# Performance work log

Measured on AMD Instinct MI355X. Metric: run time of the kernel, lower is better.

## Reference

```python
import jax, jax.numpy as jnp
import numpy as np

NUM_CLASSES = 81
BACKGROUND = 0
TOP_K = 200
KEEP_TOP_K = 200
CONF_THR = 0.01
NMS_THR = 0.45
B = 32
P = 24564  # SSD512 prior count


def setup_inputs() -> dict:
    key = jax.random.key(0)
    k1, k2, kc, ks = jax.random.split(key, 4)
    loc_data = jax.random.normal(k1, (B, P * 4), jnp.float32) * 0.5
    conf_data = jax.random.uniform(k2, (B, P * NUM_CLASSES), dtype=jnp.float32)
    # priors in corner form [xmin,ymin,xmax,ymax] within [0,1], plus Caffe-style variances
    ctr = jax.random.uniform(kc, (P, 2), minval=0.05, maxval=0.95, dtype=jnp.float32)
    sz = jax.random.uniform(ks, (P, 2), minval=0.02, maxval=0.30, dtype=jnp.float32)
    pboxes = jnp.concatenate([ctr - sz * 0.5, ctr + sz * 0.5], axis=1)  # [P,4]
    variances = jnp.tile(jnp.array([0.1, 0.1, 0.2, 0.2], jnp.float32), (P, 1))  # [P,4]
    prior_data = jnp.stack([pboxes, variances], axis=0).reshape(1, 2, P * 4)
    return {"loc_data": loc_data, "conf_data": conf_data, "prior_data": prior_data}


def _decode(loc, priors, variances):
    # CENTER_SIZE decode, Caffe DetectionOutput convention (priors in corner form).
    pw = priors[:, 2] - priors[:, 0]
    ph = priors[:, 3] - priors[:, 1]
    pcx = (priors[:, 0] + priors[:, 2]) * 0.5
    pcy = (priors[:, 1] + priors[:, 3]) * 0.5
    cx = variances[:, 0] * loc[:, 0] * pw + pcx
    cy = variances[:, 1] * loc[:, 1] * ph + pcy
    w = jnp.exp(variances[:, 2] * loc[:, 2]) * pw
    h = jnp.exp(variances[:, 3] * loc[:, 3]) * ph
    return jnp.stack([cx - w * 0.5, cy - h * 0.5, cx + w * 0.5, cy + h * 0.5], axis=-1)


def _pairwise_iou(b):  # [K,4] -> [K,K]
    x1 = jnp.maximum(b[:, None, 0], b[None, :, 0])
    y1 = jnp.maximum(b[:, None, 1], b[None, :, 1])
    x2 = jnp.minimum(b[:, None, 2], b[None, :, 2])
    y2 = jnp.minimum(b[:, None, 3], b[None, :, 3])
    inter = jnp.clip(x2 - x1, 0.0) * jnp.clip(y2 - y1, 0.0)
    area = jnp.clip(b[:, 2] - b[:, 0], 0.0) * jnp.clip(b[:, 3] - b[:, 1], 0.0)
    union = area[:, None] + area[None, :] - inter
    return inter / jnp.maximum(union, 1e-10)


def _nms_one_class(scores, boxes):
    # scores: [P], boxes: [P,4] -> kept scores [TOP_K], candidate boxes [TOP_K,4]
    s = jnp.where(scores > CONF_THR, scores, -1.0)
    vals, idx = jax.lax.top_k(s, TOP_K)
    cand = boxes[idx]                      # [TOP_K,4]
    iou = _pairwise_iou(cand)              # [TOP_K,TOP_K]
    valid = vals > CONF_THR

    def body(i, carry):
        keep, suppressed = carry
        is_kept = valid[i] & jnp.logical_not(suppressed[i])
        keep = keep.at[i].set(is_kept)
        suppressed = suppressed | (is_kept & (iou[i] > NMS_THR))
        return keep, suppressed

    keep, _ = jax.lax.fori_loop(
        0, TOP_K, body,
        (jnp.zeros((TOP_K,), jnp.bool_), jnp.zeros((TOP_K,), jnp.bool_)))
    kept_scores = jnp.where(keep, vals, 0.0)
    return kept_scores, cand


def _detection_output(loc_data, conf_data, prior_data):
    bsz = loc_data.shape[0]
    nprior = loc_data.shape[1] // 4
    loc = loc_data.reshape(bsz, nprior, 4)
    conf = conf_data.reshape(bsz, nprior, NUM_CLASSES).transpose(0, 2, 1)  # [B,C,P]
    pr = prior_data.reshape(2, nprior, 4)
    priors, variances = pr[0], pr[1]

    decoded = jax.vmap(lambda l: _decode(l, priors, variances))(loc)  # [B,P,4]

    # kill background class
    bg = (jnp.arange(NUM_CLASSES) == BACKGROUND)[None, :, None]
    conf = jnp.where(bg, -1.0, conf)

    nms_bc = jax.vmap(jax.vmap(_nms_one_class, in_axes=(0, None)), in_axes=(0, 0))
    scores, cboxes = nms_bc(conf, decoded)  # [B,C,TOP_K], [B,C,TOP_K,4]

    flat_s = scores.reshape(bsz, NUM_CLASSES * TOP_K)
    top_s, top_i = jax.lax.top_k(flat_s, KEEP_TOP_K)          # [B,KEEP]
    labels = (top_i // TOP_K).astype(jnp.float32)
    flat_b = cboxes.reshape(bsz, NUM_CLASSES * TOP_K, 4)
    top_b = jnp.take_along_axis(flat_b, top_i[..., None], axis=1)  # [B,KEEP,4]

    img_id = jnp.broadcast_to(
        jnp.arange(bsz, dtype=jnp.float32)[:, None], (bsz, KEEP_TOP_K))
    rows = jnp.concatenate(
        [img_id[..., None], labels[..., None], top_s[..., None], top_b], axis=-1)
    rows = jnp.where((top_s > 0.0)[..., None], rows, 0.0)
    return rows[:, None, :, :]  # [B,1,KEEP_TOP_K,7]


def reference(loc_data, conf_data, prior_data):
    return _detection_output(loc_data, conf_data, prior_data)
```

## Files before the change

### kernel.cpp

```cpp
#include <hip/hip_runtime.h>
#include <stdint.h>

typedef uint32_t u32;
typedef uint64_t u64;
typedef uint16_t u16;

#define NCLS 81
#define TOPK 200
#define KEEPK 200
#define CONF_THR 0.01f
#define NMS_THR 0.45f
#define NB 32
#define NP 24564
#define NFLAT (NCLS * TOPK)
#define NPCHUNK 256
#define NCHUNK ((NP + NPCHUNK - 1) / NPCHUNK)
#define CAP 512
#define NBC (NB * NCLS)
#define NGRP (NBC / 4)
#define LCAP 16
#define THRF 0.98828125f

__device__ __forceinline__ u32 fkey(float f) {
  u32 u = __float_as_uint(f);
  return (u & 0x80000000u) ? ~u : (u | 0x80000000u);
}
__device__ __forceinline__ float unfkey(u32 k) {
  u32 u = (k & 0x80000000u) ? (k & 0x7FFFFFFFu) : ~k;
  return __uint_as_float(u);
}

__global__ __launch_bounds__(256) void collect_cands(const float* __restrict__ conf,
                                                     u32* __restrict__ lcnt,
                                                     u64* __restrict__ lcand) {
  __shared__ u32 cnt81[NCLS];
  __shared__ u64 stage[NCLS * LCAP];

  const int tid = threadIdx.x;
  const int blk = blockIdx.x;
  const int b = blk / NCHUNK, chunk = blk % NCHUNK;
  const int p0 = chunk * NPCHUNK;
  const int cntp = min(NPCHUNK, NP - p0);
  const int tot4 = (cntp * NCLS) >> 2;
  const float4* __restrict__ src = (const float4*)(conf + ((size_t)b * NP + p0) * NCLS);

  for (int i = tid; i < NCLS; i += 256) cnt81[i] = 0u;
  __syncthreads();

  auto push = [&](int f, float s) {
    u32 pi = (u32)f / (u32)NCLS;
    u32 c = (u32)f - pi * (u32)NCLS;
    if (c != 0u) {
      u32 sl = atomicAdd(&cnt81[c], 1u);
      if (sl < (u32)LCAP) {
        u32 p = (u32)p0 + pi;
        stage[c * LCAP + sl] = ((u64)fkey(s) << 32) | (u32)(~p);
      }
    }
  };
  auto proc = [&](float4 v, int i4) {
    if (v.x >= THRF) push(i4 * 4 + 0, v.x);
    if (v.y >= THRF) push(i4 * 4 + 1, v.y);
    if (v.z >= THRF) push(i4 * 4 + 2, v.z);
    if (v.w >= THRF) push(i4 * 4 + 3, v.w);
  };

  for (int i = tid; i < tot4; i += 512) {
    int i2 = i + 256;
    bool g2 = i2 < tot4;
    float4 v0 = src[i];
    float4 v1;
    if (g2) v1 = src[i2];
    proc(v0, i);
    if (g2) proc(v1, i2);
  }
  __syncthreads();

  u32* gc = lcnt + (size_t)blk * NCLS;
  for (int i = tid; i < NCLS; i += 256) gc[i] = cnt81[i];
  u64* gl = lcand + (size_t)blk * NCLS * LCAP;
  for (int i = tid; i < NCLS * LCAP; i += 256) gl[i] = stage[i];
}

__global__ __launch_bounds__(256) void perclass_v11(
    const float* __restrict__ loc, const float* __restrict__ conf,
    const float* __restrict__ prior, const u32* __restrict__ lcnt,
    const u64* __restrict__ lcand, float* __restrict__ kept,
    float* __restrict__ cbox) {
  __shared__ u64 cand4[4][CAP + 17];
  __shared__ u32 hist[256];
  __shared__ u32 ck4[4][96], offs4[4][96];
  __shared__ u32 sscan[256];
  __shared__ float bx0[4][TOPK], bx1[4][TOPK], bx2[4][TOPK], bx3[4][TOPK];
  __shared__ float barea4[4][TOPK], bscore4[4][TOPK];
  __shared__ u32 nv[4], flagv[4];
  __shared__ u32 s_sel, s_rem, s_cnt, s_cnt2;

  const int tid = threadIdx.x;
  int i0 = blockIdx.x;
  int grp = (i0 & 7) * (NGRP / 8) + (i0 >> 3);

  if (tid < 4) flagv[tid] = 0u;
  __syncthreads();

  for (int t = tid; t < 384; t += 256) {
    int g = t / 96, chunk = t - g * 96;
    int bc = 4 * grp + g;
    int b = bc / NCLS, c = bc - b * NCLS;
    u32 m = 0u;
    if (c != 0) m = lcnt[(size_t)(b * NCHUNK + chunk) * NCLS + c];
    ck4[g][chunk] = m;
    if (m > (u32)LCAP) atomicOr(&flagv[g], 1u);
  }
  __syncthreads();

  for (int r = 0; r < 2; ++r) {
    int g = r * 2 + (tid >> 7);
    int ln = tid & 127;
    sscan[tid] = (ln < 96) ? ck4[g][ln] : 0u;
    __syncthreads();
    for (int d = 1; d < 128; d <<= 1) {
      u32 add = (ln >= d) ? sscan[tid - d] : 0u;
      __syncthreads();
      sscan[tid] += add;
      __syncthreads();
    }
    if (ln < 96) offs4[g][ln] = sscan[tid] - ck4[g][ln];
    if (ln == 95) nv[g] = sscan[tid];
    __syncthreads();
  }

  for (int i = tid; i < CAP; i += 256) {
    cand4[0][i] = 0ull; cand4[1][i] = 0ull; cand4[2][i] = 0ull; cand4[3][i] = 0ull;
  }
  __syncthreads();
  for (int t = tid; t < 384; t += 256) {
    int g = t / 96, chunk = t - g * 96;
    int bc = 4 * grp + g;
    int b = bc / NCLS, c = bc - b * NCLS;
    u32 n = nv[g];
    bool fast = (flagv[g] == 0u) && n >= (u32)TOPK && n <= (u32)CAP && c != 0;
    if (fast) {
      const u64* srcl = lcand + ((size_t)(b * NCHUNK + chunk) * NCLS + c) * LCAP;
      u32 o = offs4[g][chunk], m = ck4[g][chunk];
      for (u32 j = 0; j < m; ++j) cand4[g][o + j] = srcl[j];
    }
  }
  __syncthreads();

  for (int g = 0; g < 4; ++g) {
    int bc = 4 * grp + g;
    int b = bc / NCLS, c = bc - b * NCLS;
    u32 n = nv[g];
    bool fast = (flagv[g] == 0u) && n >= (u32)TOPK && n <= (u32)CAP;
    if (c == 0 || fast) continue;
    const float* confb = conf + (size_t)b * NP * NCLS + c;
    auto loadscore = [&](int p) -> float {
      float s = confb[(size_t)p * NCLS];
      return (s > CONF_THR) ? s : -1.0f;
    };
    u32 pfx = 0, K = TOPK;
    for (int shift = 24; shift >= 0; shift -= 8) {
      hist[tid] = 0; __syncthreads();
      u32 himask = (shift == 24) ? 0u : (0xFFFFFFFFu << (shift + 8));
      for (int p = tid; p < NP; p += 256) {
        u32 kf = fkey(loadscore(p));
        if ((kf & himask) == pfx) atomicAdd(&hist[(kf >> shift) & 255u], 1u);
      }
      __syncthreads();
      if (tid == 0) {
        u32 rem = K;
        int bin = 255;
        for (; bin > 0; --bin) {
          u32 cv = hist[bin];
          if (cv >= rem) break;
          rem -= cv;
        }
        s_sel = (u32)bin; s_rem = rem;
      }
      __syncthreads();
      pfx |= s_sel << shift; K = s_rem;
    }
    const u32 T = pfx;
    const u32 G = TOPK - K;
    cand4[g][tid] = 0ull; cand4[g][tid + 256] = 0ull;
    if (tid == 0) { s_cnt = 0; s_cnt2 = 0; }
    __syncthreads();
    for (int p = tid; p < NP; p += 256) {
      u32 kf = fkey(loadscore(p));
      if (kf > T) {
        u32 slot = atomicAdd(&s_cnt, 1u);
        cand4[g][slot] = ((u64)kf << 32) | (u32)(~(u32)p);
      } else if (kf == T) {
        u32 t2 = atomicAdd(&s_cnt2, 1u);
        u32 slot = G + t2;
        if (slot < (u32)CAP) cand4[g][slot] = ((u64)kf << 32) | (u32)(~(u32)p);
      }
    }
    __syncthreads();
  }

  {
    const int w = tid >> 6, ln = tid & 63;
    u64* cd = cand4[w];
    for (u32 k = 2; k <= 512; k <<= 1) {
      for (u32 j = k >> 1; j > 0; j >>= 1) {
        for (int pi = ln; pi < 256; pi += 64) {
          u32 l = (((u32)pi & ~(j - 1)) << 1) | ((u32)pi & (j - 1));
          u32 m = l + j;
          u64 a = cd[l], bb = cd[m];
          if (((l & k) == 0) ? (a < bb) : (a > bb)) { cd[l] = bb; cd[m] = a; }
        }
        __syncthreads();
      }
    }
  }

  {
    const int w = tid >> 6, ln = tid & 63;
    int bc = 4 * grp + w;
    int b = bc / NCLS, c = bc - b * NCLS;
    size_t keptBase = (size_t)bc * TOPK;
    if (c == 0) {
      for (int idx = ln; idx < TOPK; idx += 64) {
        kept[keptBase + idx] = 0.f;
        float* bp = cbox + (keptBase + idx) * 4;
        bp[0] = 0.f; bp[1] = 0.f; bp[2] = 0.f; bp[3] = 0.f;
      }
    } else {
      for (int idx = ln; idx < TOPK; idx += 64) {
        u64 e = cand4[w][idx];
        float myscore = unfkey((u32)(e >> 32));
        int p = (int)(~(u32)e);
        const float* lp = loc + ((size_t)b * NP + p) * 4;
        const float* pp = prior + (size_t)p * 4;
        const float* vp = prior + (size_t)NP * 4 + (size_t)p * 4;
        float p0 = pp[0], p1 = pp[1], p2 = pp[2], p3 = pp[3];
        float pw = p2 - p0, ph = p3 - p1;
        float pcx = (p0 + p2) * 0.5f, pcy = (p1 + p3) * 0.5f;
        float cx = vp[0] * lp[0] * pw + pcx;
        float cy = vp[1] * lp[1] * ph + pcy;
        float ww = expf(vp[2] * lp[2]) * pw;
        float hh = expf(vp[3] * lp[3]) * ph;
        float rx0 = cx - ww * 0.5f, ry0 = cy - hh * 0.5f;
        float rx1 = cx + ww * 0.5f, ry1 = cy + hh * 0.5f;
        bx0[w][idx] = rx0; bx1[w][idx] = ry0; bx2[w][idx] = rx1; bx3[w][idx] = ry1;
        barea4[w][idx] = fmaxf(rx1 - rx0, 0.f) * fmaxf(ry1 - ry0, 0.f);
        bscore4[w][idx] = myscore;
        float* bp = cbox + (keptBase + idx) * 4;
        bp[0] = rx0; bp[1] = ry0; bp[2] = rx1; bp[3] = ry1;
      }
    }
  }
  __syncthreads();

  {
    const int w = tid >> 6, lane = tid & 63;
    int bc = 4 * grp + w;
    int c = bc - (bc / NCLS) * NCLS;
    size_t keptBase = (size_t)bc * TOPK;
    if (c != 0) {
      float sx0[4], sy0[4], sx1[4], sy1[4], sar[4];
#pragma unroll
      for (int s = 0; s < 4; ++s) {
        int cc2 = s * 64 + lane;
        if (cc2 < TOPK) {
          sx0[s] = bx0[w][cc2]; sy0[s] = bx1[w][cc2];
          sx1[s] = bx2[w][cc2]; sy1[s] = bx3[w][cc2];
          sar[s] = barea4[w][cc2];
        } else {
          sx0[s] = 0.f; sy0[s] = 0.f; sx1[s] = 0.f; sy1[s] = 0.f; sar[s] = 0.f;
        }
      }
      u64 sup0 = 0, sup1 = 0, sup2 = 0, sup3 = 0;
      u64 kp0 = 0, kp1 = 0, kp2 = 0, kp3 = 0;

#define IOUBAL(S, OUT) { \
        float xx1 = fmaxf(a0, sx0[S]), yy1 = fmaxf(a1, sy0[S]); \
        float xx2 = fminf(a2, sx1[S]), yy2 = fminf(a3, sy1[S]); \
        float inter = fmaxf(xx2 - xx1, 0.f) * fmaxf(yy2 - yy1, 0.f); \
        float uni = aa + sar[S] - inter; \
        float iou = inter / fmaxf(uni, 1e-10f); \
        OUT = __ballot(iou > NMS_THR); }

#define NMSWORD(SWI, SUPV, KPV, JMAX) \
      for (int j = 0; j < (JMAX); ++j) { \
        int i = (SWI) * 64 + j; \
        float sc_i = bscore4[w][i]; \
        bool kept_i = (sc_i > CONF_THR) && !(((SUPV) >> j) & 1ull); \
        if (kept_i) { \
          (KPV) |= (1ull << j); \
          float a0 = bx0[w][i], a1 = bx1[w][i], a2 = bx2[w][i], a3 = bx3[w][i]; \
          float aa = barea4[w][i]; \
          u64 bb0, bb1, bb2, bb3; \
          IOUBAL(0, bb0) IOUBAL(1, bb1) IOUBAL(2, bb2) IOUBAL(3, bb3) \
          sup0 |= bb0; sup1 |= bb1; sup2 |= bb2; sup3 |= bb3; \
        } \
      }

      NMSWORD(0, sup0, kp0, 64)
      NMSWORD(1, sup1, kp1, 64)
      NMSWORD(2, sup2, kp2, 64)
      NMSWORD(3, sup3, kp3, TOPK - 192)
#undef NMSWORD
#undef IOUBAL

      {
        int cc2 = 0 * 64 + lane;
        kept[keptBase + cc2] = ((kp0 >> lane) & 1ull) ? bscore4[w][cc2] : 0.f;
      }
      {
        int cc2 = 1 * 64 + lane;
        kept[keptBase + cc2] = ((kp1 >> lane) & 1ull) ? bscore4[w][cc2] : 0.f;
      }
      {
        int cc2 = 2 * 64 + lane;
        kept[keptBase + cc2] = ((kp2 >> lane) & 1ull) ? bscore4[w][cc2] : 0.f;
      }
      {
        int cc2 = 3 * 64 + lane;
        if (cc2 < TOPK)
          kept[keptBase + cc2] = ((kp3 >> lane) & 1ull) ? bscore4[w][cc2] : 0.f;
      }
    }
  }
}

__global__ __launch_bounds__(256) void perclass_fallback(
    const float* __restrict__ loc, const float* __restrict__ conf,
    const float* __restrict__ prior, float* __restrict__ kept,
    float* __restrict__ cbox) {
  __shared__ u16 skey[NP];
  __shared__ unsigned int hist[256];
  __shared__ u64 keys[256];
  __shared__ float bx0[TOPK], bx1[TOPK], bx2[TOPK], bx3[TOPK];
  __shared__ float barea[TOPK], bscore[TOPK];
  __shared__ unsigned char sup[TOPK], keepf[TOPK];
  __shared__ unsigned int s_sel, s_rem, s_cnt, s_cnt2;

  const int tid = threadIdx.x;
  const int nwg = NB * NCLS;
  int i0 = blockIdx.x;
  int bc = (i0 & 7) * (nwg / 8) + (i0 >> 3);
  const int b = bc / NCLS, c = bc % NCLS;
  const size_t keptBase = (size_t)bc * TOPK;

  if (c == 0) {
    for (int k = tid; k < TOPK; k += 256) {
      kept[keptBase + k] = 0.f;
      float* bp = cbox + (keptBase + k) * 4;
      bp[0] = 0.f; bp[1] = 0.f; bp[2] = 0.f; bp[3] = 0.f;
    }
    return;
  }

  const float* confb = conf + (size_t)b * NP * NCLS + c;
  auto loadscore = [&](int p) -> float {
    float s = confb[(size_t)p * NCLS];
    return (s > CONF_THR) ? s : -1.0f;
  };

  for (int p = tid; p < NP; p += 256)
    skey[p] = (u16)(fkey(loadscore(p)) >> 16);
  __syncthreads();

  auto select_bin = [&](u32 Kin) {
    if (tid == 0) {
      u32 rem = Kin;
      int bin = 255;
      for (; bin > 0; --bin) {
        u32 cnt = hist[bin];
        if (cnt >= rem) break;
        rem -= cnt;
      }
      s_sel = (u32)bin; s_rem = rem;
    }
    __syncthreads();
  };

  const u32 NEGK16 = 0x407Fu;
  u32 K = TOPK;
  hist[tid] = 0; __syncthreads();
  for (int p = tid; p < NP; p += 256) atomicAdd(&hist[skey[p] >> 8], 1u);
  __syncthreads();
  select_bin(K);
  u32 pfx16 = s_sel << 8; K = s_rem;

  hist[tid] = 0; __syncthreads();
  {
    u32 hb = pfx16 >> 8;
    for (int p = tid; p < NP; p += 256) {
      u16 v = skey[p];
      if ((u32)(v >> 8) == hb) atomicAdd(&hist[v & 255], 1u);
    }
  }
  __syncthreads();
  select_bin(K);
  pfx16 |= s_sel; K = s_rem;

  const bool fillMode = (pfx16 == NEGK16);
  u32 T;
  if (!fillMode) {
    u32 pfull = pfx16 << 16;
    hist[tid] = 0; __syncthreads();
    for (int p = tid; p < NP; p += 256) {
      if ((u32)skey[p] == pfx16) {
        u32 kf = fkey(loadscore(p));
        atomicAdd(&hist[(kf >> 8) & 255], 1u);
      }
    }
    __syncthreads();
    select_bin(K);
    pfull |= s_sel << 8; K = s_rem;

    hist[tid] = 0; __syncthreads();
    for (int p = tid; p < NP; p += 256) {
      if ((u32)skey[p] == pfx16) {
        u32 kf = fkey(loadscore(p));
        if ((kf >> 8) == (pfull >> 8)) atomicAdd(&hist[kf & 255], 1u);
      }
    }
    __syncthreads();
    select_bin(K);
    T = pfull | s_sel; K = s_rem;
  } else {
    T = 0x407FFFFFu;
  }

  const u32 G = TOPK - K;
  keys[tid] = 0;
  if (tid == 0) { s_cnt = 0; s_cnt2 = 0; }
  __syncthreads();
  for (int p = tid; p < NP; p += 256) {
    u32 v = skey[p];
    if (v > pfx16) {
      float s = loadscore(p);
      u32 slot = atomicAdd(&s_cnt, 1u);
      keys[slot] = ((u64)fkey(s) << 32) | (u32)(~(u32)p);
    } else if (!fillMode && v == pfx16) {
      float s = loadscore(p);
      u32 kf = fkey(s);
      if (kf > T) {
        u32 slot = atomicAdd(&s_cnt, 1u);
        keys[slot] = ((u64)kf << 32) | (u32)(~(u32)p);
      } else if (kf == T) {
        u32 t2 = atomicAdd(&s_cnt2, 1u);
        u32 slot = G + t2;
        if (slot < 256u) keys[slot] = ((u64)kf << 32) | (u32)(~(u32)p);
      }
    }
  }
  __syncthreads();
  if (fillMode) {
    for (int k = (int)G + tid; k < TOPK; k += 256)
      keys[k] = ((u64)T << 32) | 0xFFFFFFFFull;
  }
  __syncthreads();

  for (u32 kk = 2; kk <= 256; kk <<= 1) {
    for (u32 j = kk >> 1; j > 0; j >>= 1) {
      u32 ixj = (u32)tid ^ j;
      if (ixj > (u32)tid) {
        u64 a = keys[tid], bb = keys[ixj];
        bool asc = (tid & kk) != 0;
        if (asc ? (a > bb) : (a < bb)) { keys[tid] = bb; keys[ixj] = a; }
      }
      __syncthreads();
    }
  }

  if (tid < TOPK) {
    u64 e = keys[tid];
    float s = unfkey((u32)(e >> 32));
    int p = (int)(~(u32)e);
    const float* lp = loc + ((size_t)b * NP + p) * 4;
    const float* pp = prior + (size_t)p * 4;
    const float* vp = prior + (size_t)NP * 4 + (size_t)p * 4;
    float p0 = pp[0], p1 = pp[1], p2 = pp[2], p3 = pp[3];
    float pw = p2 - p0, ph = p3 - p1;
    float pcx = (p0 + p2) * 0.5f, pcy = (p1 + p3) * 0.5f;
    float cx = vp[0] * lp[0] * pw + pcx;
    float cy = vp[1] * lp[1] * ph + pcy;
    float w = expf(vp[2] * lp[2]) * pw;
    float h = expf(vp[3] * lp[3]) * ph;
    float x0 = cx - w * 0.5f, y0 = cy - h * 0.5f;
    float x1 = cx + w * 0.5f, y1 = cy + h * 0.5f;
    bx0[tid] = x0; bx1[tid] = y0; bx2[tid] = x1; bx3[tid] = y1;
    barea[tid] = fmaxf(x1 - x0, 0.f) * fmaxf(y1 - y0, 0.f);
    bscore[tid] = s;
    sup[tid] = 0;
    keepf[tid] = 0;
  }
  __syncthreads();

  for (int i = 0; i < TOPK; ++i) {
    bool kept_i = (bscore[i] > CONF_THR) && (sup[i] == 0);
    __syncthreads();
    if (kept_i) {
      if (tid < TOPK) {
        float xx1 = fmaxf(bx0[i], bx0[tid]);
        float yy1 = fmaxf(bx1[i], bx1[tid]);
        float xx2 = fminf(bx2[i], bx2[tid]);
        float yy2 = fminf(bx3[i], bx3[tid]);
        float inter = fmaxf(xx2 - xx1, 0.f) * fmaxf(yy2 - yy1, 0.f);
        float uni = barea[i] + barea[tid] - inter;
        float iou = inter / fmaxf(uni, 1e-10f);
        if (iou > NMS_THR) sup[tid] = 1;
      }
      if (tid == 0) keepf[i] = 1;
    }
    __syncthreads();
  }

  if (tid < TOPK) {
    kept[keptBase + tid] = keepf[tid] ? bscore[tid] : 0.f;
    float* bp = cbox + (keptBase + tid) * 4;
    bp[0] = bx0[tid]; bp[1] = bx1[tid]; bp[2] = bx2[tid]; bp[3] = bx3[tid];
  }
}

__global__ __launch_bounds__(256) void final_topk(
    const float* __restrict__ kept, const float* __restrict__ cbox,
    float* __restrict__ out) {
  __shared__ u32 histm[4 * 257];
  __shared__ u32 ssuf[256];
  __shared__ u64 keys[256];
  __shared__ u32 s_sel, s_rem, s_cnt, s_cnt2;

  const int tid = threadIdx.x;
  const int b = blockIdx.x;
  const float* sc = kept + (size_t)b * NFLAT;
  const int sub4 = (tid & 3) * 257;

  auto select256s = [&](u32 Kin) {
    __syncthreads();
    u32 cntv = histm[tid] + histm[257 + tid] + histm[514 + tid] + histm[771 + tid];
    ssuf[tid] = cntv;
    __syncthreads();
    for (int d = 1; d < 256; d <<= 1) {
      u32 add = (tid + d < 256) ? ssuf[tid + d] : 0u;
      __syncthreads();
      ssuf[tid] += add;
      __syncthreads();
    }
    u32 s = ssuf[tid], above = s - cntv;
    if (s >= Kin && above < Kin) { s_sel = (u32)tid; s_rem = Kin - above; }
    __syncthreads();
  };

  u32 pfx = 0;
  u32 K = KEEPK;
  for (int shift = 24; shift >= 0; shift -= 8) {
    for (int j = tid; j < 4 * 257; j += 256) histm[j] = 0u;
    __syncthreads();
    u32 himask = (shift == 24) ? 0u : (0xFFFFFFFFu << (shift + 8));
    for (int p = tid; p < NFLAT; p += 256) {
      u32 kf = fkey(sc[p]);
      if ((kf & himask) == pfx) atomicAdd(&histm[sub4 + ((kf >> shift) & 255u)], 1u);
    }
    select256s(K);
    pfx |= s_sel << shift; K = s_rem;
  }

  const bool fill2 = (pfx == fkey(0.0f));
  const u32 G = KEEPK - K;
  keys[tid] = 0;
  if (tid == 0) { s_cnt = 0; s_cnt2 = 0; }
  __syncthreads();
  for (int p = tid; p < NFLAT; p += 256) {
    u32 kf = fkey(sc[p]);
    if (kf > pfx) {
      u32 slot = atomicAdd(&s_cnt, 1u);
      keys[slot] = ((u64)kf << 32) | (u32)(~(u32)p);
    } else if (!fill2 && kf == pfx) {
      u32 t2 = atomicAdd(&s_cnt2, 1u);
      u32 slot = G + t2;
      if (slot < 256u) keys[slot] = ((u64)kf << 32) | (u32)(~(u32)p);
    }
  }
  __syncthreads();
  if (fill2) {
    for (int k = (int)G + tid; k < KEEPK; k += 256)
      keys[k] = ((u64)pfx << 32) | 0xFFFFFFFFull;
  }
  __syncthreads();

  for (u32 kk = 2; kk <= 256; kk <<= 1) {
    for (u32 j = kk >> 1; j > 0; j >>= 1) {
      u32 ixj = (u32)tid ^ j;
      if (ixj > (u32)tid) {
        u64 a = keys[tid], bb = keys[ixj];
        bool asc = (tid & kk) != 0;
        if (asc ? (a > bb) : (a < bb)) { keys[tid] = bb; keys[ixj] = a; }
      }
      __syncthreads();
    }
  }

  if (tid < KEEPK) {
    u64 e = keys[tid];
    float s = unfkey((u32)(e >> 32));
    u32 fi = ~(u32)e;
    float r0 = 0.f, r1 = 0.f, r2 = 0.f, r3 = 0.f, r4 = 0.f, r5 = 0.f, r6 = 0.f;
    if (s > 0.f) {
      r0 = (float)b;
      r1 = (float)(fi / TOPK);
      r2 = s;
      const float* bp = cbox + ((size_t)b * NFLAT + fi) * 4;
      r3 = bp[0]; r4 = bp[1]; r5 = bp[2]; r6 = bp[3];
    }
    float* op = out + ((size_t)b * KEEPK + tid) * 7;
    op[0] = r0; op[1] = r1; op[2] = r2; op[3] = r3;
    op[4] = r4; op[5] = r5; op[6] = r6;
  }
}

extern "C" void kernel_launch(void* const* d_in, const int* in_sizes, int n_in,
                              void* d_out, int out_size, void* d_ws, size_t ws_size,
                              hipStream_t stream) {
  const float* loc = (const float*)d_in[0];
  const float* conf = (const float*)d_in[1];
  const float* prior = (const float*)d_in[2];
  float* out = (float*)d_out;

  float* kept = (float*)d_ws;
  float* cbox = kept + (size_t)NBC * TOPK;
  const size_t baseBytes = (size_t)NBC * TOPK * 5 * sizeof(float);
  const size_t lcntBytes = (size_t)NB * NCHUNK * NCLS * sizeof(u32);
  const size_t lcandBytes = (size_t)NB * NCHUNK * NCLS * LCAP * sizeof(u64);

  if (ws_size >= baseBytes + lcntBytes + lcandBytes) {
    u32* lcnt = (u32*)((char*)d_ws + baseBytes);
    u64* lcand = (u64*)((char*)d_ws + baseBytes + lcntBytes);
    collect_cands<<<dim3(NB * NCHUNK), dim3(256), 0, stream>>>(conf, lcnt, lcand);
    perclass_v11<<<dim3(NGRP), dim3(256), 0, stream>>>(loc, conf, prior, lcnt,
                                                       lcand, kept, cbox);
  } else {
    perclass_fallback<<<dim3(NBC), dim3(256), 0, stream>>>(loc, conf, prior,
                                                           kept, cbox);
  }
  final_topk<<<dim3(NB), dim3(256), 0, stream>>>(kept, cbox, out);
}
```

Measured before the change: 258.9 us.

## Split per-class NMS into a separate single-wave kernel and parallelize candidate gather

The selection kernel now stops after decoding the top boxes and writes their scores and coordinates to global memory. A new 64-thread kernel, one block per batch-class pair, then runs the ballot-based NMS. The candidate copy loop is also spread across threads per element instead of one thread looping per chunk. Splitting the work frees shared memory and lets many small NMS blocks run in parallel rather than four serialized in one block, at the cost of an extra launch and a global round trip for boxes and scores.

```diff
diff --git a/kernel.cpp b/kernel.cpp
--- a/kernel.cpp
+++ b/kernel.cpp
@@ -82,17 +82,15 @@
   for (int i = tid; i < NCLS * LCAP; i += 256) gl[i] = stage[i];
 }
 
-__global__ __launch_bounds__(256) void perclass_v11(
+__global__ __launch_bounds__(256) void perclass_sel(
     const float* __restrict__ loc, const float* __restrict__ conf,
     const float* __restrict__ prior, const u32* __restrict__ lcnt,
-    const u64* __restrict__ lcand, float* __restrict__ kept,
+    const u64* __restrict__ lcand, float* __restrict__ bscoreg,
     float* __restrict__ cbox) {
   __shared__ u64 cand4[4][CAP + 17];
   __shared__ u32 hist[256];
   __shared__ u32 ck4[4][96], offs4[4][96];
   __shared__ u32 sscan[256];
-  __shared__ float bx0[4][TOPK], bx1[4][TOPK], bx2[4][TOPK], bx3[4][TOPK];
-  __shared__ float barea4[4][TOPK], bscore4[4][TOPK];
   __shared__ u32 nv[4], flagv[4];
   __shared__ u32 s_sel, s_rem, s_cnt, s_cnt2;
 
@@ -134,16 +132,18 @@
     cand4[0][i] = 0ull; cand4[1][i] = 0ull; cand4[2][i] = 0ull; cand4[3][i] = 0ull;
   }
   __syncthreads();
-  for (int t = tid; t < 384; t += 256) {
-    int g = t / 96, chunk = t - g * 96;
+  for (int t = tid; t < 4 * 96 * LCAP; t += 256) {
+    int j = t & (LCAP - 1);
+    int rest = t >> 4;
+    int chunk = rest % 96;
+    int g = rest / 96;
     int bc = 4 * grp + g;
     int b = bc / NCLS, c = bc - b * NCLS;
     u32 n = nv[g];
     bool fast = (flagv[g] == 0u) && n >= (u32)TOPK && n <= (u32)CAP && c != 0;
-    if (fast) {
+    if (fast && (u32)j < ck4[g][chunk]) {
       const u64* srcl = lcand + ((size_t)(b * NCHUNK + chunk) * NCLS + c) * LCAP;
-      u32 o = offs4[g][chunk], m = ck4[g][chunk];
-      for (u32 j = 0; j < m; ++j) cand4[g][o + j] = srcl[j];
+      cand4[g][offs4[g][chunk] + j] = srcl[j];
     }
   }
   __syncthreads();
@@ -216,113 +216,114 @@
     }
   }
 
-  {
-    const int w = tid >> 6, ln = tid & 63;
-    int bc = 4 * grp + w;
+  for (int t = tid; t < 4 * TOPK; t += 256) {
+    int g = t / TOPK, idx = t - g * TOPK;
+    int bc = 4 * grp + g;
     int b = bc / NCLS, c = bc - b * NCLS;
-    size_t keptBase = (size_t)bc * TOPK;
+    size_t base = (size_t)bc * TOPK + idx;
     if (c == 0) {
-      for (int idx = ln; idx < TOPK; idx += 64) {
-        kept[keptBase + idx] = 0.f;
-        float* bp = cbox + (keptBase + idx) * 4;
-        bp[0] = 0.f; bp[1] = 0.f; bp[2] = 0.f; bp[3] = 0.f;
-      }
+      bscoreg[base] = -1.0f;
+      float* bp = cbox + base * 4;
+      bp[0] = 0.f; bp[1] = 0.f; bp[2] = 0.f; bp[3] = 0.f;
     } else {
-      for (int idx = ln; idx < TOPK; idx += 64) {
-        u64 e = cand4[w][idx];
-        float myscore = unfkey((u32)(e >> 32));
-        int p = (int)(~(u32)e);
-        const float* lp = loc + ((size_t)b * NP + p) * 4;
-        const float* pp = prior + (size_t)p * 4;
-        const float* vp = prior + (size_t)NP * 4 + (size_t)p * 4;
-        float p0 = pp[0], p1 = pp[1], p2 = pp[2], p3 = pp[3];
-        float pw = p2 - p0, ph = p3 - p1;
-        float pcx = (p0 + p2) * 0.5f, pcy = (p1 + p3) * 0.5f;
-        float cx = vp[0] * lp[0] * pw + pcx;
-        float cy = vp[1] * lp[1] * ph + pcy;
-        float ww = expf(vp[2] * lp[2]) * pw;
-        float hh = expf(vp[3] * lp[3]) * ph;
-        float rx0 = cx - ww * 0.5f, ry0 = cy - hh * 0.5f;
-        float rx1 = cx + ww * 0.5f, ry1 = cy + hh * 0.5f;
-        bx0[w][idx] = rx0; bx1[w][idx] = ry0; bx2[w][idx] = rx1; bx3[w][idx] = ry1;
-        barea4[w][idx] = fmaxf(rx1 - rx0, 0.f) * fmaxf(ry1 - ry0, 0.f);
-        bscore4[w][idx] = myscore;
-        float* bp = cbox + (keptBase + idx) * 4;
-        bp[0] = rx0; bp[1] = ry0; bp[2] = rx1; bp[3] = ry1;
-      }
-    }
-  }
-  __syncthreads();
-
-  {
-    const int w = tid >> 6, lane = tid & 63;
-    int bc = 4 * grp + w;
-    int c = bc - (bc / NCLS) * NCLS;
-    size_t keptBase = (size_t)bc * TOPK;
-    if (c != 0) {
-      float sx0[4], sy0[4], sx1[4], sy1[4], sar[4];
+      u64 e = cand4[g][idx];
+      float myscore = unfkey((u32)(e >> 32));
+      int p = (int)(~(u32)e);
+      const float* lp = loc + ((size_t)b * NP + p) * 4;
+      const float* pp = prior + (size_t)p * 4;
+      const float* vp = prior + (size_t)NP * 4 + (size_t)p * 4;
+      float p0 = pp[0], p1 = pp[1], p2 = pp[2], p3 = pp[3];
+      float pw = p2 - p0, ph = p3 - p1;
+      float pcx = (p0 + p2) * 0.5f, pcy = (p1 + p3) * 0.5f;
+      float cx = vp[0] * lp[0] * pw + pcx;
+      float cy = vp[1] * lp[1] * ph + pcy;
+      float ww = expf(vp[2] * lp[2]) * pw;
+      float hh = expf(vp[3] * lp[3]) * ph;
+      float rx0 = cx - ww * 0.5f, ry0 = cy - hh * 0.5f;
+      float rx1 = cx + ww * 0.5f, ry1 = cy + hh * 0.5f;
+      bscoreg[base] = myscore;
+      float* bp = cbox + base * 4;
+      bp[0] = rx0; bp[1] = ry0; bp[2] = rx1; bp[3] = ry1;
+    }
+  }
+}
+
+__global__ __launch_bounds__(64) void nms_kernel(const float* __restrict__ cbox,
+                                                 const float* __restrict__ bscoreg,
+                                                 float* __restrict__ kept) {
+  __shared__ float bx0[TOPK], bx1[TOPK], bx2[TOPK], bx3[TOPK];
+  __shared__ float barea[TOPK], bscore[TOPK];
+
+  const int bc = blockIdx.x;
+  const int lane = threadIdx.x;
+  const size_t base = (size_t)bc * TOPK;
+
+  float sx0[4], sy0[4], sx1[4], sy1[4], sar[4];
 #pragma unroll
-      for (int s = 0; s < 4; ++s) {
-        int cc2 = s * 64 + lane;
-        if (cc2 < TOPK) {
-          sx0[s] = bx0[w][cc2]; sy0[s] = bx1[w][cc2];
-          sx1[s] = bx2[w][cc2]; sy1[s] = bx3[w][cc2];
-          sar[s] = barea4[w][cc2];
-        } else {
-          sx0[s] = 0.f; sy0[s] = 0.f; sx1[s] = 0.f; sy1[s] = 0.f; sar[s] = 0.f;
-        }
-      }
-      u64 sup0 = 0, sup1 = 0, sup2 = 0, sup3 = 0;
-      u64 kp0 = 0, kp1 = 0, kp2 = 0, kp3 = 0;
+  for (int s = 0; s < 4; ++s) {
+    int cc2 = s * 64 + lane;
+    if (cc2 < TOPK) {
+      float4 bb = *reinterpret_cast<const float4*>(cbox + (base + cc2) * 4);
+      float sc = bscoreg[base + cc2];
+      float ar = fmaxf(bb.z - bb.x, 0.f) * fmaxf(bb.w - bb.y, 0.f);
+      sx0[s] = bb.x; sy0[s] = bb.y; sx1[s] = bb.z; sy1[s] = bb.w; sar[s] = ar;
+      bx0[cc2] = bb.x; bx1[cc2] = bb.y; bx2[cc2] = bb.z; bx3[cc2] = bb.w;
+      barea[cc2] = ar; bscore[cc2] = sc;
+    } else {
+      sx0[s] = 0.f; sy0[s] = 0.f; sx1[s] = 0.f; sy1[s] = 0.f; sar[s] = 0.f;
+    }
+  }
+  __syncthreads();
+
+  u64 sup0 = 0, sup1 = 0, sup2 = 0, sup3 = 0;
+  u64 kp0 = 0, kp1 = 0, kp2 = 0, kp3 = 0;
 
 #define IOUBAL(S, OUT) { \
-        float xx1 = fmaxf(a0, sx0[S]), yy1 = fmaxf(a1, sy0[S]); \
-        float xx2 = fminf(a2, sx1[S]), yy2 = fminf(a3, sy1[S]); \
-        float inter = fmaxf(xx2 - xx1, 0.f) * fmaxf(yy2 - yy1, 0.f); \
-        float uni = aa + sar[S] - inter; \
-        float iou = inter / fmaxf(uni, 1e-10f); \
-        OUT = __ballot(iou > NMS_THR); }
+    float xx1 = fmaxf(a0, sx0[S]), yy1 = fmaxf(a1, sy0[S]); \
+    float xx2 = fminf(a2, sx1[S]), yy2 = fminf(a3, sy1[S]); \
+    float inter = fmaxf(xx2 - xx1, 0.f) * fmaxf(yy2 - yy1, 0.f); \
+    float uni = aa + sar[S] - inter; \
+    float iou = inter / fmaxf(uni, 1e-10f); \
+    OUT = __ballot(iou > NMS_THR); }
 
 #define NMSWORD(SWI, SUPV, KPV, JMAX) \
-      for (int j = 0; j < (JMAX); ++j) { \
-        int i = (SWI) * 64 + j; \
-        float sc_i = bscore4[w][i]; \
-        bool kept_i = (sc_i > CONF_THR) && !(((SUPV) >> j) & 1ull); \
-        if (kept_i) { \
-          (KPV) |= (1ull << j); \
-          float a0 = bx0[w][i], a1 = bx1[w][i], a2 = bx2[w][i], a3 = bx3[w][i]; \
-          float aa = barea4[w][i]; \
-          u64 bb0, bb1, bb2, bb3; \
-          IOUBAL(0, bb0) IOUBAL(1, bb1) IOUBAL(2, bb2) IOUBAL(3, bb3) \
-          sup0 |= bb0; sup1 |= bb1; sup2 |= bb2; sup3 |= bb3; \
-        } \
-      }
-
-      NMSWORD(0, sup0, kp0, 64)
-      NMSWORD(1, sup1, kp1, 64)
-      NMSWORD(2, sup2, kp2, 64)
-      NMSWORD(3, sup3, kp3, TOPK - 192)
+  for (int j = 0; j < (JMAX); ++j) { \
+    int i = (SWI) * 64 + j; \
+    float sc_i = bscore[i]; \
+    bool kept_i = (sc_i > CONF_THR) && !(((SUPV) >> j) & 1ull); \
+    if (kept_i) { \
+      (KPV) |= (1ull << j); \
+      float a0 = bx0[i], a1 = bx1[i], a2 = bx2[i], a3 = bx3[i]; \
+      float aa = barea[i]; \
+      u64 bb0, bb1, bb2, bb3; \
+      IOUBAL(0, bb0) IOUBAL(1, bb1) IOUBAL(2, bb2) IOUBAL(3, bb3) \
+      sup0 |= bb0; sup1 |= bb1; sup2 |= bb2; sup3 |= bb3; \
+    } \
+  }
+
+  NMSWORD(0, sup0, kp0, 64)
+  NMSWORD(1, sup1, kp1, 64)
+  NMSWORD(2, sup2, kp2, 64)
+  NMSWORD(3, sup3, kp3, TOPK - 192)
 #undef NMSWORD
 #undef IOUBAL
 
-      {
-        int cc2 = 0 * 64 + lane;
-        kept[keptBase + cc2] = ((kp0 >> lane) & 1ull) ? bscore4[w][cc2] : 0.f;
-      }
-      {
-        int cc2 = 1 * 64 + lane;
-        kept[keptBase + cc2] = ((kp1 >> lane) & 1ull) ? bscore4[w][cc2] : 0.f;
-      }
-      {
-        int cc2 = 2 * 64 + lane;
-        kept[keptBase + cc2] = ((kp2 >> lane) & 1ull) ? bscore4[w][cc2] : 0.f;
-      }
-      {
-        int cc2 = 3 * 64 + lane;
-        if (cc2 < TOPK)
-          kept[keptBase + cc2] = ((kp3 >> lane) & 1ull) ? bscore4[w][cc2] : 0.f;
-      }
-    }
+  {
+    int cc2 = 0 * 64 + lane;
+    kept[base + cc2] = ((kp0 >> lane) & 1ull) ? bscore[cc2] : 0.f;
+  }
+  {
+    int cc2 = 1 * 64 + lane;
+    kept[base + cc2] = ((kp1 >> lane) & 1ull) ? bscore[cc2] : 0.f;
+  }
+  {
+    int cc2 = 2 * 64 + lane;
+    kept[base + cc2] = ((kp2 >> lane) & 1ull) ? bscore[cc2] : 0.f;
+  }
+  {
+    int cc2 = 3 * 64 + lane;
+    if (cc2 < TOPK)
+      kept[base + cc2] = ((kp3 >> lane) & 1ull) ? bscore[cc2] : 0.f;
   }
 }
 
@@ -628,13 +629,16 @@
   const size_t baseBytes = (size_t)NBC * TOPK * 5 * sizeof(float);
   const size_t lcntBytes = (size_t)NB * NCHUNK * NCLS * sizeof(u32);
   const size_t lcandBytes = (size_t)NB * NCHUNK * NCLS * LCAP * sizeof(u64);
-
-  if (ws_size >= baseBytes + lcntBytes + lcandBytes) {
+  const size_t bscBytes = (size_t)NBC * TOPK * sizeof(float);
+
+  if (ws_size >= baseBytes + lcntBytes + lcandBytes + bscBytes) {
     u32* lcnt = (u32*)((char*)d_ws + baseBytes);
     u64* lcand = (u64*)((char*)d_ws + baseBytes + lcntBytes);
+    float* bscoreg = (float*)((char*)d_ws + baseBytes + lcntBytes + lcandBytes);
     collect_cands<<<dim3(NB * NCHUNK), dim3(256), 0, stream>>>(conf, lcnt, lcand);
-    perclass_v11<<<dim3(NGRP), dim3(256), 0, stream>>>(loc, conf, prior, lcnt,
-                                                       lcand, kept, cbox);
+    perclass_sel<<<dim3(NGRP), dim3(256), 0, stream>>>(loc, conf, prior, lcnt,
+                                                       lcand, bscoreg, cbox);
+    nms_kernel<<<dim3(NBC), dim3(64), 0, stream>>>(cbox, bscoreg, kept);
   } else {
     perclass_fallback<<<dim3(NBC), dim3(256), 0, stream>>>(loc, conf, prior,
                                                            kept, cbox);
```

After: 265.9 us. +2.7%, slower.
